# Kernel optimization log

Measured on AMD Instinct MI355X. Metric: run time of the kernel, lower is better.

The kernel has to match this reference:

```python
import jax, jax.numpy as jnp
import numpy as np

EMB_DIM = 768
N_HEAD = 12
WIN = (14, 14)  # relative_window_size; seq_len must equal 14*14=196
BATCH = 64
SEQ = WIN[0] * WIN[1]


def _relative_position_index(wh, ww):
    coords = np.stack(np.meshgrid(np.arange(wh), np.arange(ww), indexing='ij'))
    coords = coords.reshape(2, -1)
    rel = coords[:, :, None] - coords[:, None, :]          # [2, S, S]
    rel = rel.transpose(1, 2, 0).astype(np.int32)          # [S, S, 2]
    rel[:, :, 0] += wh - 1
    rel[:, :, 1] += ww - 1
    rel[:, :, 0] *= 2 * ww - 1
    return rel.sum(-1)                                     # [S, S]


def setup_inputs() -> dict:
    key = jax.random.key(0)
    ks = jax.random.split(key, 10)
    d = EMB_DIM
    std = 0.01
    x = jax.random.normal(ks[0], (BATCH, SEQ, d), dtype=jnp.float32)
    Wq = std * jax.random.normal(ks[1], (d, d), dtype=jnp.float32)
    Wk = std * jax.random.normal(ks[2], (d, d), dtype=jnp.float32)
    Wv = std * jax.random.normal(ks[3], (d, d), dtype=jnp.float32)
    Wo = std * jax.random.normal(ks[4], (d, d), dtype=jnp.float32)
    bq = jnp.zeros((d,), jnp.float32)
    bk = jnp.zeros((d,), jnp.float32)
    bv = jnp.zeros((d,), jnp.float32)
    bo = jnp.zeros((d,), jnp.float32)
    n_bias = (2 * WIN[0] - 1) * (2 * WIN[1] - 1)           # 729
    bias_table = std * jax.random.normal(ks[5], (n_bias, N_HEAD), dtype=jnp.float32)
    rel_index = jnp.asarray(_relative_position_index(WIN[0], WIN[1]))  # int32 [S,S]
    return {"x": x, "Wq": Wq, "bq": bq, "Wk": Wk, "bk": bk, "Wv": Wv,
            "bv": bv, "Wo": Wo, "bo": bo, "bias_table": bias_table,
            "rel_index": rel_index}


def reference(x, Wq, bq, Wk, bk, Wv, bv, Wo, bo, bias_table, rel_index):
    B, S, D = x.shape
    H = N_HEAD
    pd = D // H  # projection_dim

    def split_heads(t):
        return t.reshape(B, S, H, pd).transpose(0, 2, 1, 3)  # [B,H,S,pd]

    q = split_heads(x @ Wq + bq)
    k = split_heads(x @ Wk + bk)
    v = split_heads(x @ Wv + bv)

    # scores: [B,H,S,S], scaled by sqrt(projection_dim) as in the source
    score = jnp.einsum('bhqd,bhkd->bhqk', q, k) / jnp.sqrt(jnp.float32(pd))

    # Swin-style relative position bias: gather [S*S] rows -> [1,H,S,S]
    bias = bias_table[rel_index.reshape(-1)].reshape(S, S, H)
    bias = bias.transpose(2, 0, 1)[None]
    score = score + bias

    weight = jax.nn.softmax(score, axis=-1)
    out = jnp.einsum('bhqk,bhkd->bhqd', weight, v)          # [B,H,S,pd]
    out = out.transpose(0, 2, 1, 3).reshape(B, S, D)
    return out @ Wo + bo
```

## Files before the change

### kernel.cpp

```cpp
#include <hip/hip_runtime.h>
#include <hip/hip_bf16.h>


typedef __bf16 bf16x8 __attribute__((ext_vector_type(8)));
typedef __bf16 bf16x4 __attribute__((ext_vector_type(4)));
typedef float  f32x4  __attribute__((ext_vector_type(4)));

#define MROWS 12544
#define DDIM  768
#define NHEAD 12
#define SEQ   196
#define KSTR  72
#define VSTR  232

static __device__ __forceinline__ f32x4 MFMA(bf16x8 a, bf16x8 b, f32x4 c) {
    return __builtin_amdgcn_mfma_f32_16x16x32_bf16(a, b, c, 0, 0, 0);
}

static __device__ __forceinline__ void gload16(const __bf16* g, __bf16* l) {
    __builtin_amdgcn_global_load_lds(
        (const __attribute__((address_space(1))) void*)(g),
        (__attribute__((address_space(3))) void*)(l),
        16, 0, 0);
}

__global__ __launch_bounds__(256) void f2b(const float* __restrict__ in,
                                           __bf16* __restrict__ out) {
    size_t i = ((size_t)blockIdx.x * 256 + threadIdx.x) * 8;
    f32x4 a = *(const f32x4*)&in[i];
    f32x4 b = *(const f32x4*)&in[i + 4];
    bf16x8 o;
    o[0] = (__bf16)a[0]; o[1] = (__bf16)a[1]; o[2] = (__bf16)a[2]; o[3] = (__bf16)a[3];
    o[4] = (__bf16)b[0]; o[5] = (__bf16)b[1]; o[6] = (__bf16)b[2]; o[7] = (__bf16)b[3];
    *(bf16x8*)&out[i] = o;
}

__global__ __launch_bounds__(256) void wtrans(const float* __restrict__ W0, const float* __restrict__ W1,
                                              const float* __restrict__ W2, const float* __restrict__ W3,
                                              __bf16* __restrict__ T0, __bf16* __restrict__ T1,
                                              __bf16* __restrict__ T2, __bf16* __restrict__ T3) {
    const float* Ws[4] = {W0, W1, W2, W3};
    __bf16*      Ts[4] = {T0, T1, T2, T3};
    const float* W = Ws[blockIdx.z];
    __bf16*      T = Ts[blockIdx.z];
    __shared__ __bf16 t[32][33];
    int k0 = blockIdx.x * 32, n0 = blockIdx.y * 32;
    int c = threadIdx.x & 31, r = threadIdx.x >> 5;
#pragma unroll
    for (int i = 0; i < 4; ++i)
        t[r + i * 8][c] = (__bf16)W[(size_t)(k0 + r + i * 8) * DDIM + n0 + c];
    __syncthreads();
#pragma unroll
    for (int i = 0; i < 4; ++i)
        T[(size_t)(n0 + r + i * 8) * DDIM + k0 + c] = t[c][r + i * 8];
}

__global__ __launch_bounds__(256) void bias_pre(const float* __restrict__ table,
                                                const int* __restrict__ rel,
                                                __bf16* __restrict__ biasH) {
    int i = blockIdx.x * 256 + threadIdx.x;
    if (i < NHEAD * SEQ * SEQ) {
        int h = i / (SEQ * SEQ), qk = i - h * (SEQ * SEQ);
        biasH[i] = (__bf16)table[rel[qk] * NHEAD + h];
    }
}

template <typename OutT, int NMAT>
__global__ __launch_bounds__(512, 2) void gemm8p(const __bf16* __restrict__ A,
                                                 const __bf16* __restrict__ Bt,
                                                 const float* __restrict__ bz0,
                                                 const float* __restrict__ bz1,
                                                 const float* __restrict__ bz2,
                                                 OutT* __restrict__ Cz0,
                                                 OutT* __restrict__ Cz1,
                                                 OutT* __restrict__ Cz2,
                                                 int nbn) {
    __shared__ __bf16 As[3][256 * 64];
    __shared__ __bf16 Bs[2][256 * 64];

    const int nwg = gridDim.x, orig = blockIdx.x;
    const int qq = nwg >> 3, r8 = nwg & 7, xcd = orig & 7, lin = orig >> 3;
    const int wg = (xcd < r8 ? xcd * (qq + 1) : r8 * (qq + 1) + (xcd - r8) * qq) + lin;
    const int bm = wg / nbn, bn = wg - bm * nbn;
    const int m0 = bm * 256, n0g = bn * 256;

    const int tid = threadIdx.x, w = tid >> 6, l = tid & 63;
    const int lr = l & 15, lg = l >> 4;
    const int wrow = (w >> 2) * 128;
    const int wcol = (w & 3) * 64;

    const int srow = w * 8 + (l >> 3);
    const int scol = ((l & 7) ^ ((l >> 3) & 7)) * 8;
    const __bf16* gA = A  + (size_t)(m0 + srow) * DDIM + scol;
    const __bf16* gB = Bt + (size_t)(n0g + srow) * DDIM + scol;

#define STAGE_A(slot, h, kt)                                                      \
    do {                                                                          \
        gload16(gA + ((h) * 128 + 0) * DDIM + (kt) * 64,                          \
                &As[slot][(h) * 8192 + 0 + w * 512]);                             \
        gload16(gA + ((h) * 128 + 64) * DDIM + (kt) * 64,                         \
                &As[slot][(h) * 8192 + 4096 + w * 512]);                          \
    } while (0)
#define STAGE_B(slot, h, kt)                                                      \
    do {                                                                          \
        gload16(gB + ((h) * 128 + 0) * DDIM + (kt) * 64,                          \
                &Bs[slot][(h) * 8192 + 0 + w * 512]);                             \
        gload16(gB + ((h) * 128 + 64) * DDIM + (kt) * 64,                         \
                &Bs[slot][(h) * 8192 + 4096 + w * 512]);                          \
    } while (0)

#define AF(slot, mf, ks)                                                          \
    (*(const bf16x8*)&As[slot][(w >> 2) * 8192 + ((mf) * 16 + lr) * 64 +          \
                              ((((ks) * 4 + lg) ^ (lr & 7))) * 8])
#define BF(slot, nf, ks)                                                          \
    (*(const bf16x8*)&Bs[slot][((w & 3) >> 1) * 8192 +                            \
                              ((w & 1) * 64 + (nf) * 16 + lr) * 64 +              \
                              ((((ks) * 4 + lg) ^ (lr & 7))) * 8])

    f32x4 acc[8][4];
#pragma unroll
    for (int i = 0; i < 8; ++i)
#pragma unroll
        for (int j = 0; j < 4; ++j) acc[i][j] = (f32x4){0.f, 0.f, 0.f, 0.f};

    bf16x8 a0, a1, a2, a3;
    bf16x8 bfr00, bfr01, bfr10, bfr11, bfr20, bfr21, bfr30, bfr31;

#define DSLOAD_A(slot, mf0)                                                       \
    a0 = AF(slot, mf0, 0); a1 = AF(slot, mf0, 1);                                 \
    a2 = AF(slot, (mf0) + 1, 0); a3 = AF(slot, (mf0) + 1, 1);
#define DSLOAD_B(slot)                                                            \
    bfr00 = BF(slot, 0, 0); bfr01 = BF(slot, 0, 1);                               \
    bfr10 = BF(slot, 1, 0); bfr11 = BF(slot, 1, 1);                               \
    bfr20 = BF(slot, 2, 0); bfr21 = BF(slot, 2, 1);                               \
    bfr30 = BF(slot, 3, 0); bfr31 = BF(slot, 3, 1);
#define BARRIER_IN()                                                              \
    __builtin_amdgcn_sched_barrier(0);                                            \
    __builtin_amdgcn_s_barrier();                                                 \
    asm volatile("s_waitcnt lgkmcnt(0)" ::: "memory");                            \
    __builtin_amdgcn_sched_barrier(0);                                            \
    __builtin_amdgcn_s_setprio(1);
#define BARRIER_OUT()                                                             \
    __builtin_amdgcn_s_setprio(0);                                                \
    __builtin_amdgcn_sched_barrier(0);                                            \
    __builtin_amdgcn_s_barrier();                                                 \
    __builtin_amdgcn_sched_barrier(0);
#define MFMACL(mf0)                                                               \
    acc[mf0][0] = MFMA(a0, bfr00, acc[mf0][0]);                                   \
    acc[mf0][0] = MFMA(a1, bfr01, acc[mf0][0]);                                   \
    acc[(mf0) + 1][0] = MFMA(a2, bfr00, acc[(mf0) + 1][0]);                       \
    acc[(mf0) + 1][0] = MFMA(a3, bfr01, acc[(mf0) + 1][0]);                       \
    acc[mf0][1] = MFMA(a0, bfr10, acc[mf0][1]);                                   \
    acc[mf0][1] = MFMA(a1, bfr11, acc[mf0][1]);                                   \
    acc[(mf0) + 1][1] = MFMA(a2, bfr10, acc[(mf0) + 1][1]);                       \
    acc[(mf0) + 1][1] = MFMA(a3, bfr11, acc[(mf0) + 1][1]);                       \
    acc[mf0][2] = MFMA(a0, bfr20, acc[mf0][2]);                                   \
    acc[mf0][2] = MFMA(a1, bfr21, acc[mf0][2]);                                   \
    acc[(mf0) + 1][2] = MFMA(a2, bfr20, acc[(mf0) + 1][2]);                       \
    acc[(mf0) + 1][2] = MFMA(a3, bfr21, acc[(mf0) + 1][2]);                       \
    acc[mf0][3] = MFMA(a0, bfr30, acc[mf0][3]);                                   \
    acc[mf0][3] = MFMA(a1, bfr31, acc[mf0][3]);                                   \
    acc[(mf0) + 1][3] = MFMA(a2, bfr30, acc[(mf0) + 1][3]);                       \
    acc[(mf0) + 1][3] = MFMA(a3, bfr31, acc[(mf0) + 1][3]);

    STAGE_A(0, 0, 0); STAGE_A(0, 1, 0); STAGE_B(0, 0, 0); STAGE_B(0, 1, 0);
    STAGE_A(1, 0, 1); STAGE_A(1, 1, 1); STAGE_B(1, 0, 1); STAGE_B(1, 1, 1);
    asm volatile("s_waitcnt vmcnt(8)" ::: "memory");
    __builtin_amdgcn_s_barrier();
    __builtin_amdgcn_sched_barrier(0);

#pragma unroll
    for (int i = 0; i < 6; ++i) {
        const int s0 = (2 * i) % 3, s1 = (2 * i + 1) % 3, s2 = (2 * i + 2) % 3;
        DSLOAD_A(s0, 0); DSLOAD_B(0);
        if (i < 5) STAGE_A(s2, 0, 2 * i + 2);
        BARRIER_IN(); MFMACL(0); BARRIER_OUT();
        DSLOAD_A(s0, 2);
        if (i < 5) STAGE_A(s2, 1, 2 * i + 2);
        BARRIER_IN(); MFMACL(2); BARRIER_OUT();
        DSLOAD_A(s0, 4);
        if (i < 5) STAGE_B(0, 0, 2 * i + 2);
        BARRIER_IN(); MFMACL(4); BARRIER_OUT();
        DSLOAD_A(s0, 6);
        if (i < 5) {
            STAGE_B(0, 1, 2 * i + 2);
            asm volatile("s_waitcnt vmcnt(8)" ::: "memory");
        } else {
            asm volatile("s_waitcnt vmcnt(0)" ::: "memory");
        }
        BARRIER_IN(); MFMACL(6); BARRIER_OUT();
        DSLOAD_A(s1, 0); DSLOAD_B(1);
        if (i < 5) STAGE_A(s0, 0, 2 * i + 3);
        BARRIER_IN(); MFMACL(0); BARRIER_OUT();
        DSLOAD_A(s1, 2);
        if (i < 5) STAGE_A(s0, 1, 2 * i + 3);
        BARRIER_IN(); MFMACL(2); BARRIER_OUT();
        DSLOAD_A(s1, 4);
        if (i < 5) STAGE_B(1, 0, 2 * i + 3);
        BARRIER_IN(); MFMACL(4); BARRIER_OUT();
        DSLOAD_A(s1, 6);
        if (i < 5) {
            STAGE_B(1, 1, 2 * i + 3);
            asm volatile("s_waitcnt vmcnt(8)" ::: "memory");
        }
        BARRIER_IN(); MFMACL(6); BARRIER_OUT();
    }

    const int mat = (NMAT == 1) ? 0 : (n0g / DDIM);
    const int colbase = n0g - mat * DDIM + wcol;
    const float* bz = (mat == 0) ? bz0 : (mat == 1 ? bz1 : bz2);
    OutT* Cc = (mat == 0) ? Cz0 : (mat == 1 ? Cz1 : Cz2);
#pragma unroll
    for (int nf = 0; nf < 4; ++nf) {
        const int col = colbase + nf * 16 + lr;
        const float bb = bz[col];
#pragma unroll
        for (int mf = 0; mf < 8; ++mf) {
            const int row = m0 + wrow + mf * 16 + lg * 4;
#pragma unroll
            for (int r2 = 0; r2 < 4; ++r2)
                Cc[(size_t)(row + r2) * DDIM + col] = (OutT)(acc[mf][nf][r2] + bb);
        }
    }
#undef STAGE_A
#undef STAGE_B
#undef AF
#undef BF
#undef DSLOAD_A
#undef DSLOAD_B
#undef BARRIER_IN
#undef BARRIER_OUT
#undef MFMACL
}

__global__ __launch_bounds__(512, 2) void attn_kernel(const __bf16* __restrict__ Qg,
                                                      const __bf16* __restrict__ Kg,
                                                      const __bf16* __restrict__ Vg,
                                                      const __bf16* __restrict__ biasH,
                                                      __bf16* __restrict__ Og) {
    __shared__ __bf16 Ksm[208 * KSTR];
    __shared__ __bf16 Vts[64 * VSTR];
    __shared__ __bf16 Psm[8 * 16 * VSTR];

    const int b = blockIdx.x, h = blockIdx.y;
    const int tid = threadIdx.x, w = tid >> 6, l = tid & 63;
    const int lr = l & 15, lg = l >> 4;
    const size_t base = (size_t)(b * SEQ) * DDIM + h * 64;
    const __bf16* Kb = Kg + base;
    const __bf16* Vb = Vg + base;
    const __bf16* Qb = Qg + base;
    const __bf16* bh = biasH + (size_t)h * (SEQ * SEQ);

    for (int c = tid; c < SEQ * 8; c += 512) {
        int kk = c >> 3, d8 = (c & 7) << 3;
        *(bf16x8*)&Ksm[kk * KSTR + d8] = *(const bf16x8*)&Kb[(size_t)kk * DDIM + d8];
    }
    for (int c = tid; c < 12 * 9; c += 512) {
        int kk = SEQ + c / 9, d8 = (c % 9) * 8;
        *(uint4*)&Ksm[kk * KSTR + d8] = make_uint4(0u, 0u, 0u, 0u);
    }
    for (int c = tid; c < SEQ * 8; c += 512) {
        int kk = c >> 3, d8 = (c & 7) << 3;
        bf16x8 vv = *(const bf16x8*)&Vb[(size_t)kk * DDIM + d8];
#pragma unroll
        for (int j = 0; j < 8; ++j) Vts[(d8 + j) * VSTR + kk] = vv[j];
    }
    for (int c = tid; c < 64 * 28; c += 512)
        Vts[(c / 28) * VSTR + SEQ + (c % 28)] = (__bf16)0.f;
    __bf16* Pw = &Psm[w * 16 * VSTR];
    for (int c = l; c < 256; c += 64)
        Pw[(c >> 4) * VSTR + 208 + (c & 15)] = (__bf16)0.f;
    __syncthreads();

    for (int qt = w; qt < 13; qt += 8) {
        const int q0 = qt * 16;
        const int q = q0 + lr;
        const int qrow = min(q, SEQ - 1);
        bf16x8 bq0 = *(const bf16x8*)&Qb[(size_t)qrow * DDIM + lg * 8];
        bf16x8 bq1 = *(const bf16x8*)&Qb[(size_t)qrow * DDIM + 32 + lg * 8];

        f32x4 sc[13];
        __builtin_amdgcn_s_setprio(1);
#pragma unroll
        for (int t = 0; t < 13; ++t) {
            bf16x8 kf0 = *(const bf16x8*)&Ksm[(t * 16 + lr) * KSTR + lg * 8];
            bf16x8 kf1 = *(const bf16x8*)&Ksm[(t * 16 + lr) * KSTR + 32 + lg * 8];
            f32x4 a = {0.f, 0.f, 0.f, 0.f};
            a = MFMA(kf0, bq0, a);
            a = MFMA(kf1, bq1, a);
            sc[t] = a;
        }
        __builtin_amdgcn_s_setprio(0);

        float mx = -1e30f;
#pragma unroll
        for (int t = 0; t < 13; ++t) {
            const bool val4 = (t < 12) || (lg == 0);
            float bb[4] = {0.f, 0.f, 0.f, 0.f};
            if (val4) {
                bf16x4 b4 = *(const bf16x4*)&bh[(size_t)qrow * SEQ + t * 16 + lg * 4];
#pragma unroll
                for (int r = 0; r < 4; ++r) bb[r] = (float)b4[r];
            }
#pragma unroll
            for (int r = 0; r < 4; ++r) {
                float v = val4 ? (sc[t][r] * 0.125f + bb[r]) : -1e30f;
                sc[t][r] = v;
                mx = fmaxf(mx, v);
            }
        }
        mx = fmaxf(mx, __shfl_xor(mx, 16));
        mx = fmaxf(mx, __shfl_xor(mx, 32));

        float sum = 0.f;
#pragma unroll
        for (int t = 0; t < 13; ++t)
#pragma unroll
            for (int r = 0; r < 4; ++r) {
                float p = __expf(sc[t][r] - mx);
                sum += p;
                sc[t][r] = p;
            }
        sum += __shfl_xor(sum, 16);
        sum += __shfl_xor(sum, 32);
        const float inv = 1.f / sum;

#pragma unroll
        for (int t = 0; t < 13; ++t) {
            bf16x4 pk;
#pragma unroll
            for (int r = 0; r < 4; ++r) pk[r] = (__bf16)sc[t][r];
            *(bf16x4*)&Pw[lr * VSTR + t * 16 + lg * 4] = pk;
        }

        f32x4 oa[4];
#pragma unroll
        for (int i = 0; i < 4; ++i) oa[i] = (f32x4){0.f, 0.f, 0.f, 0.f};
        __builtin_amdgcn_s_setprio(1);
#pragma unroll
        for (int kt = 0; kt < 7; ++kt) {
            bf16x8 pf = *(const bf16x8*)&Pw[lr * VSTR + kt * 32 + lg * 8];
#pragma unroll
            for (int nt = 0; nt < 4; ++nt) {
                bf16x8 vf = *(const bf16x8*)&Vts[(nt * 16 + lr) * VSTR + kt * 32 + lg * 8];
                oa[nt] = MFMA(vf, pf, oa[nt]);
            }
        }
        __builtin_amdgcn_s_setprio(0);

        if (q < SEQ) {
#pragma unroll
            for (int nt = 0; nt < 4; ++nt) {
                bf16x4 ok;
#pragma unroll
                for (int r = 0; r < 4; ++r) ok[r] = (__bf16)(oa[nt][r] * inv);
                *(bf16x4*)&Og[(size_t)(b * SEQ + q) * DDIM + h * 64 + nt * 16 + lg * 4] = ok;
            }
        }
    }
}

extern "C" void kernel_launch(void* const* d_in, const int* in_sizes, int n_in,
                              void* d_out, int out_size, void* d_ws, size_t ws_size,
                              hipStream_t stream) {
    const float* x     = (const float*)d_in[0];
    const float* Wq    = (const float*)d_in[1];
    const float* bq    = (const float*)d_in[2];
    const float* Wk    = (const float*)d_in[3];
    const float* bk    = (const float*)d_in[4];
    const float* Wv    = (const float*)d_in[5];
    const float* bv    = (const float*)d_in[6];
    const float* Wo    = (const float*)d_in[7];
    const float* bo    = (const float*)d_in[8];
    const float* table = (const float*)d_in[9];
    const int*   rel   = (const int*)d_in[10];
    float* out = (float*)d_out;

    char* ws = (char*)d_ws;
    auto alloc = [&](size_t bytes) {
        char* p = ws;
        ws += (bytes + 255) & ~(size_t)255;
        return p;
    };
    const size_t mat = (size_t)MROWS * DDIM * sizeof(__bf16);
    __bf16* xb    = (__bf16*)alloc(mat);
    __bf16* Tqkv  = (__bf16*)alloc((size_t)3 * DDIM * DDIM * 2);
    __bf16* To    = (__bf16*)alloc((size_t)DDIM * DDIM * 2);
    __bf16* Qb    = (__bf16*)alloc(mat);
    __bf16* Kb    = (__bf16*)alloc(mat);
    __bf16* Vb    = (__bf16*)alloc(mat);
    __bf16* AO    = (__bf16*)alloc(mat);
    __bf16* biasH = (__bf16*)alloc((size_t)NHEAD * SEQ * SEQ * 2);

    f2b<<<dim3(4704), 256, 0, stream>>>(x, xb);
    wtrans<<<dim3(24, 24, 4), 256, 0, stream>>>(Wq, Wk, Wv, Wo,
                                                Tqkv, Tqkv + (size_t)DDIM * DDIM,
                                                Tqkv + (size_t)2 * DDIM * DDIM, To);
    bias_pre<<<dim3(1801), 256, 0, stream>>>(table, rel, biasH);

    gemm8p<__bf16, 3><<<dim3(441), 512, 0, stream>>>(xb, Tqkv, bq, bk, bv,
                                                     Qb, Kb, Vb, 9);
    attn_kernel<<<dim3(64, 12), 512, 0, stream>>>(Qb, Kb, Vb, biasH, AO);
    gemm8p<float, 1><<<dim3(147), 512, 0, stream>>>(AO, To, bo, bo, bo,
                                                    out, out, out, 3);
}
```

Measured before the change: 171.8 us.

## Split attention softmax into two online-softmax chunks and relax launch bounds

Replaces the single-pass softmax over all 13 key tiles with two chunks (8 and 5 tiles) using a running max and sum, rescaling the output accumulator between chunks. Each chunk's P tiles are written to LDS and consumed by the PV MFMAs, so fewer score registers are live at once. The launch bound minimum blocks per SM also drops from 2 to 1, giving the compiler more register headroom. The rescaling adds extra exp and multiply work and may reduce occupancy.

Result: faster. 160.2 us (-6.8%).

```diff
diff --git a/kernel.cpp b/kernel.cpp
--- a/kernel.cpp
+++ b/kernel.cpp
@@ -233,7 +233,7 @@
 #undef MFMACL
 }
 
-__global__ __launch_bounds__(512, 2) void attn_kernel(const __bf16* __restrict__ Qg,
+__global__ __launch_bounds__(512, 1) void attn_kernel(const __bf16* __restrict__ Qg,
                                                       const __bf16* __restrict__ Kg,
                                                       const __bf16* __restrict__ Vg,
                                                       const __bf16* __restrict__ biasH,
@@ -272,6 +272,77 @@
         Pw[(c >> 4) * VSTR + 208 + (c & 15)] = (__bf16)0.f;
     __syncthreads();
 
+#define CHUNK(T0, NTC, KT0, KTN)                                                  \
+    {                                                                             \
+        f32x4 sc[NTC];                                                            \
+        __builtin_amdgcn_s_setprio(1);                                            \
+        _Pragma("unroll")                                                         \
+        for (int tt = 0; tt < NTC; ++tt) {                                        \
+            const int t = (T0) + tt;                                              \
+            bf16x8 kf0 = *(const bf16x8*)&Ksm[(t * 16 + lr) * KSTR + lg * 8];     \
+            bf16x8 kf1 = *(const bf16x8*)&Ksm[(t * 16 + lr) * KSTR + 32 + lg * 8];\
+            f32x4 a = {0.f, 0.f, 0.f, 0.f};                                       \
+            a = MFMA(kf0, bq0, a);                                                \
+            a = MFMA(kf1, bq1, a);                                                \
+            sc[tt] = a;                                                           \
+        }                                                                         \
+        __builtin_amdgcn_s_setprio(0);                                            \
+        float mc = -1e30f;                                                        \
+        _Pragma("unroll")                                                         \
+        for (int tt = 0; tt < NTC; ++tt) {                                        \
+            const int t = (T0) + tt;                                              \
+            const bool val4 = (t < 12) || (lg == 0);                              \
+            float bb[4] = {0.f, 0.f, 0.f, 0.f};                                   \
+            if (val4) {                                                           \
+                bf16x4 b4 = *(const bf16x4*)&bh[(size_t)qrow * SEQ + t * 16 + lg * 4]; \
+                _Pragma("unroll")                                                 \
+                for (int r = 0; r < 4; ++r) bb[r] = (float)b4[r];                 \
+            }                                                                     \
+            _Pragma("unroll")                                                     \
+            for (int r = 0; r < 4; ++r) {                                         \
+                float v = val4 ? (sc[tt][r] * 0.125f + bb[r]) : -1e30f;           \
+                sc[tt][r] = v;                                                    \
+                mc = fmaxf(mc, v);                                                \
+            }                                                                     \
+        }                                                                         \
+        mc = fmaxf(mc, __shfl_xor(mc, 16));                                       \
+        mc = fmaxf(mc, __shfl_xor(mc, 32));                                       \
+        const float mnew = fmaxf(m_run, mc);                                      \
+        const float fsc = __expf(m_run - mnew);                                   \
+        m_run = mnew;                                                             \
+        s_run *= fsc;                                                             \
+        _Pragma("unroll")                                                         \
+        for (int i = 0; i < 4; ++i)                                               \
+            _Pragma("unroll")                                                     \
+            for (int r = 0; r < 4; ++r) oa[i][r] *= fsc;                          \
+        float ps = 0.f;                                                           \
+        _Pragma("unroll")                                                         \
+        for (int tt = 0; tt < NTC; ++tt) {                                        \
+            bf16x4 pk;                                                            \
+            _Pragma("unroll")                                                     \
+            for (int r = 0; r < 4; ++r) {                                         \
+                float p = __expf(sc[tt][r] - m_run);                              \
+                ps += p;                                                          \
+                pk[r] = (__bf16)p;                                                \
+            }                                                                     \
+            *(bf16x4*)&Pw[lr * VSTR + ((T0) + tt) * 16 + lg * 4] = pk;            \
+        }                                                                         \
+        ps += __shfl_xor(ps, 16);                                                 \
+        ps += __shfl_xor(ps, 32);                                                 \
+        s_run += ps;                                                              \
+        __builtin_amdgcn_s_setprio(1);                                            \
+        _Pragma("unroll")                                                         \
+        for (int kt = (KT0); kt < (KTN); ++kt) {                                  \
+            bf16x8 pf = *(const bf16x8*)&Pw[lr * VSTR + kt * 32 + lg * 8];        \
+            _Pragma("unroll")                                                     \
+            for (int nt = 0; nt < 4; ++nt) {                                      \
+                bf16x8 vf = *(const bf16x8*)&Vts[(nt * 16 + lr) * VSTR + kt * 32 + lg * 8]; \
+                oa[nt] = MFMA(vf, pf, oa[nt]);                                    \
+            }                                                                     \
+        }                                                                         \
+        __builtin_amdgcn_s_setprio(0);                                            \
+    }
+
     for (int qt = w; qt < 13; qt += 8) {
         const int q0 = qt * 16;
         const int q = q0 + lr;
@@ -279,75 +350,15 @@
         bf16x8 bq0 = *(const bf16x8*)&Qb[(size_t)qrow * DDIM + lg * 8];
         bf16x8 bq1 = *(const bf16x8*)&Qb[(size_t)qrow * DDIM + 32 + lg * 8];
 
-        f32x4 sc[13];
-        __builtin_amdgcn_s_setprio(1);
-#pragma unroll
-        for (int t = 0; t < 13; ++t) {
-            bf16x8 kf0 = *(const bf16x8*)&Ksm[(t * 16 + lr) * KSTR + lg * 8];
-            bf16x8 kf1 = *(const bf16x8*)&Ksm[(t * 16 + lr) * KSTR + 32 + lg * 8];
-            f32x4 a = {0.f, 0.f, 0.f, 0.f};
-            a = MFMA(kf0, bq0, a);
-            a = MFMA(kf1, bq1, a);
-            sc[t] = a;
-        }
-        __builtin_amdgcn_s_setprio(0);
-
-        float mx = -1e30f;
-#pragma unroll
-        for (int t = 0; t < 13; ++t) {
-            const bool val4 = (t < 12) || (lg == 0);
-            float bb[4] = {0.f, 0.f, 0.f, 0.f};
-            if (val4) {
-                bf16x4 b4 = *(const bf16x4*)&bh[(size_t)qrow * SEQ + t * 16 + lg * 4];
-#pragma unroll
-                for (int r = 0; r < 4; ++r) bb[r] = (float)b4[r];
-            }
-#pragma unroll
-            for (int r = 0; r < 4; ++r) {
-                float v = val4 ? (sc[t][r] * 0.125f + bb[r]) : -1e30f;
-                sc[t][r] = v;
-                mx = fmaxf(mx, v);
-            }
-        }
-        mx = fmaxf(mx, __shfl_xor(mx, 16));
-        mx = fmaxf(mx, __shfl_xor(mx, 32));
-
-        float sum = 0.f;
-#pragma unroll
-        for (int t = 0; t < 13; ++t)
-#pragma unroll
-            for (int r = 0; r < 4; ++r) {
-                float p = __expf(sc[t][r] - mx);
-                sum += p;
-                sc[t][r] = p;
-            }
-        sum += __shfl_xor(sum, 16);
-        sum += __shfl_xor(sum, 32);
-        const float inv = 1.f / sum;
-
-#pragma unroll
-        for (int t = 0; t < 13; ++t) {
-            bf16x4 pk;
-#pragma unroll
-            for (int r = 0; r < 4; ++r) pk[r] = (__bf16)sc[t][r];
-            *(bf16x4*)&Pw[lr * VSTR + t * 16 + lg * 4] = pk;
-        }
-
+        float m_run = -1e30f, s_run = 0.f;
         f32x4 oa[4];
 #pragma unroll
         for (int i = 0; i < 4; ++i) oa[i] = (f32x4){0.f, 0.f, 0.f, 0.f};
-        __builtin_amdgcn_s_setprio(1);
-#pragma unroll
-        for (int kt = 0; kt < 7; ++kt) {
-            bf16x8 pf = *(const bf16x8*)&Pw[lr * VSTR + kt * 32 + lg * 8];
-#pragma unroll
-            for (int nt = 0; nt < 4; ++nt) {
-                bf16x8 vf = *(const bf16x8*)&Vts[(nt * 16 + lr) * VSTR + kt * 32 + lg * 8];
-                oa[nt] = MFMA(vf, pf, oa[nt]);
-            }
-        }
-        __builtin_amdgcn_s_setprio(0);
-
+
+        CHUNK(0, 8, 0, 4);
+        CHUNK(8, 5, 4, 7);
+
+        const float inv = 1.f / s_run;
         if (q < SEQ) {
 #pragma unroll
             for (int nt = 0; nt < 4; ++nt) {
@@ -358,6 +369,7 @@
             }
         }
     }
+#undef CHUNK
 }
 
 extern "C" void kernel_launch(void* const* d_in, const int* in_sizes, int n_in,
```

## Chunk attention softmax online to cut registers and LDS, raise occupancy

Applied to the files above, without the earlier changes.

Splits the per-query-tile score computation into four key chunks processed with an online (running max/sum) softmax, so only 4 score tiles stay live instead of 13. The P staging buffer shrinks to a 64-wide stride and the K stride drops to 68, reducing LDS per block. Launch bounds move to 4 blocks per SM to exploit the lower register and LDS footprint. This adds rescaling work (extra exps and multiplies per chunk) and changes the K padding stride, which may alter LDS bank-conflict behavior.

New measurement: 265.9 us. +54.8%, slower.

```diff
diff --git a/kernel.cpp b/kernel.cpp
--- a/kernel.cpp
+++ b/kernel.cpp
@@ -10,8 +10,9 @@
 #define DDIM  768
 #define NHEAD 12
 #define SEQ   196
-#define KSTR  72
+#define KSTR  68
 #define VSTR  232
+#define PSTR  68
 
 static __device__ __forceinline__ f32x4 MFMA(bf16x8 a, bf16x8 b, f32x4 c) {
     return __builtin_amdgcn_mfma_f32_16x16x32_bf16(a, b, c, 0, 0, 0);
@@ -233,14 +234,92 @@
 #undef MFMACL
 }
 
-__global__ __launch_bounds__(512, 2) void attn_kernel(const __bf16* __restrict__ Qg,
+template <int T0, int NTC, int KT0, int NKT, bool REZERO>
+static __device__ __forceinline__ void attn_chunk(
+    const __bf16* Ksm, const __bf16* Vts, __bf16* Pw, const __bf16* bh,
+    int qrow, int lr, int lg, bf16x8 bq0, bf16x8 bq1,
+    float& m_run, float& s_run, f32x4* oa) {
+    f32x4 sc[NTC];
+    __builtin_amdgcn_s_setprio(1);
+#pragma unroll
+    for (int tt = 0; tt < NTC; ++tt) {
+        const int t = T0 + tt;
+        bf16x8 kf0 = *(const bf16x8*)&Ksm[(t * 16 + lr) * KSTR + lg * 8];
+        bf16x8 kf1 = *(const bf16x8*)&Ksm[(t * 16 + lr) * KSTR + 32 + lg * 8];
+        f32x4 a = {0.f, 0.f, 0.f, 0.f};
+        a = MFMA(kf0, bq0, a);
+        a = MFMA(kf1, bq1, a);
+        sc[tt] = a;
+    }
+    __builtin_amdgcn_s_setprio(0);
+    float mc = -1e30f;
+#pragma unroll
+    for (int tt = 0; tt < NTC; ++tt) {
+        const int t = T0 + tt;
+        const bool val4 = (t < 12) || (lg == 0);
+        float bb[4] = {0.f, 0.f, 0.f, 0.f};
+        if (val4) {
+            bf16x4 b4 = *(const bf16x4*)&bh[(size_t)qrow * SEQ + t * 16 + lg * 4];
+#pragma unroll
+            for (int r = 0; r < 4; ++r) bb[r] = (float)b4[r];
+        }
+#pragma unroll
+        for (int r = 0; r < 4; ++r) {
+            float v = val4 ? (sc[tt][r] * 0.125f + bb[r]) : -1e30f;
+            sc[tt][r] = v;
+            mc = fmaxf(mc, v);
+        }
+    }
+    mc = fmaxf(mc, __shfl_xor(mc, 16));
+    mc = fmaxf(mc, __shfl_xor(mc, 32));
+    const float mnew = fmaxf(m_run, mc);
+    const float fsc = __expf(m_run - mnew);
+    m_run = mnew;
+    s_run *= fsc;
+#pragma unroll
+    for (int i = 0; i < 4; ++i)
+#pragma unroll
+        for (int r = 0; r < 4; ++r) oa[i][r] *= fsc;
+    float ps = 0.f;
+#pragma unroll
+    for (int tt = 0; tt < NTC; ++tt) {
+        bf16x4 pk;
+#pragma unroll
+        for (int r = 0; r < 4; ++r) {
+            float p = __expf(sc[tt][r] - m_run);
+            ps += p;
+            pk[r] = (__bf16)p;
+        }
+        *(bf16x4*)&Pw[lr * PSTR + tt * 16 + lg * 4] = pk;
+    }
+    ps += __shfl_xor(ps, 16);
+    ps += __shfl_xor(ps, 32);
+    s_run += ps;
+    if (REZERO) {
+        bf16x4 z4 = {(__bf16)0.f, (__bf16)0.f, (__bf16)0.f, (__bf16)0.f};
+        *(bf16x4*)&Pw[lr * PSTR + 16 + lg * 4] = z4;
+    }
+    __builtin_amdgcn_s_setprio(1);
+#pragma unroll
+    for (int ktl = 0; ktl < NKT; ++ktl) {
+        bf16x8 pf = *(const bf16x8*)&Pw[lr * PSTR + ktl * 32 + lg * 8];
+#pragma unroll
+        for (int nt = 0; nt < 4; ++nt) {
+            bf16x8 vf = *(const bf16x8*)&Vts[(nt * 16 + lr) * VSTR + (KT0 + ktl) * 32 + lg * 8];
+            oa[nt] = MFMA(vf, pf, oa[nt]);
+        }
+    }
+    __builtin_amdgcn_s_setprio(0);
+}
+
+__global__ __launch_bounds__(512, 4) void attn_kernel(const __bf16* __restrict__ Qg,
                                                       const __bf16* __restrict__ Kg,
                                                       const __bf16* __restrict__ Vg,
                                                       const __bf16* __restrict__ biasH,
                                                       __bf16* __restrict__ Og) {
     __shared__ __bf16 Ksm[208 * KSTR];
     __shared__ __bf16 Vts[64 * VSTR];
-    __shared__ __bf16 Psm[8 * 16 * VSTR];
+    __shared__ __bf16 Psm[8 * 16 * PSTR];
 
     const int b = blockIdx.x, h = blockIdx.y;
     const int tid = threadIdx.x, w = tid >> 6, l = tid & 63;
@@ -255,8 +334,8 @@
         int kk = c >> 3, d8 = (c & 7) << 3;
         *(bf16x8*)&Ksm[kk * KSTR + d8] = *(const bf16x8*)&Kb[(size_t)kk * DDIM + d8];
     }
-    for (int c = tid; c < 12 * 9; c += 512) {
-        int kk = SEQ + c / 9, d8 = (c % 9) * 8;
+    for (int c = tid; c < 12 * 8; c += 512) {
+        int kk = SEQ + (c >> 3), d8 = (c & 7) << 3;
         *(uint4*)&Ksm[kk * KSTR + d8] = make_uint4(0u, 0u, 0u, 0u);
     }
     for (int c = tid; c < SEQ * 8; c += 512) {
@@ -267,10 +346,9 @@
     }
     for (int c = tid; c < 64 * 28; c += 512)
         Vts[(c / 28) * VSTR + SEQ + (c % 28)] = (__bf16)0.f;
-    __bf16* Pw = &Psm[w * 16 * VSTR];
-    for (int c = l; c < 256; c += 64)
-        Pw[(c >> 4) * VSTR + 208 + (c & 15)] = (__bf16)0.f;
     __syncthreads();
+
+    __bf16* Pw = &Psm[w * 16 * PSTR];
 
     for (int qt = w; qt < 13; qt += 8) {
         const int q0 = qt * 16;
@@ -279,75 +357,17 @@
         bf16x8 bq0 = *(const bf16x8*)&Qb[(size_t)qrow * DDIM + lg * 8];
         bf16x8 bq1 = *(const bf16x8*)&Qb[(size_t)qrow * DDIM + 32 + lg * 8];
 
-        f32x4 sc[13];
-        __builtin_amdgcn_s_setprio(1);
-#pragma unroll
-        for (int t = 0; t < 13; ++t) {
-            bf16x8 kf0 = *(const bf16x8*)&Ksm[(t * 16 + lr) * KSTR + lg * 8];
-            bf16x8 kf1 = *(const bf16x8*)&Ksm[(t * 16 + lr) * KSTR + 32 + lg * 8];
-            f32x4 a = {0.f, 0.f, 0.f, 0.f};
-            a = MFMA(kf0, bq0, a);
-            a = MFMA(kf1, bq1, a);
-            sc[t] = a;
-        }
-        __builtin_amdgcn_s_setprio(0);
-
-        float mx = -1e30f;
-#pragma unroll
-        for (int t = 0; t < 13; ++t) {
-            const bool val4 = (t < 12) || (lg == 0);
-            float bb[4] = {0.f, 0.f, 0.f, 0.f};
-            if (val4) {
-                bf16x4 b4 = *(const bf16x4*)&bh[(size_t)qrow * SEQ + t * 16 + lg * 4];
-#pragma unroll
-                for (int r = 0; r < 4; ++r) bb[r] = (float)b4[r];
-            }
-#pragma unroll
-            for (int r = 0; r < 4; ++r) {
-                float v = val4 ? (sc[t][r] * 0.125f + bb[r]) : -1e30f;
-                sc[t][r] = v;
-                mx = fmaxf(mx, v);
-            }
-        }
-        mx = fmaxf(mx, __shfl_xor(mx, 16));
-        mx = fmaxf(mx, __shfl_xor(mx, 32));
-
-        float sum = 0.f;
-#pragma unroll
-        for (int t = 0; t < 13; ++t)
-#pragma unroll
-            for (int r = 0; r < 4; ++r) {
-                float p = __expf(sc[t][r] - mx);
-                sum += p;
-                sc[t][r] = p;
-            }
-        sum += __shfl_xor(sum, 16);
-        sum += __shfl_xor(sum, 32);
-        const float inv = 1.f / sum;
-
-#pragma unroll
-        for (int t = 0; t < 13; ++t) {
-            bf16x4 pk;
-#pragma unroll
-            for (int r = 0; r < 4; ++r) pk[r] = (__bf16)sc[t][r];
-            *(bf16x4*)&Pw[lr * VSTR + t * 16 + lg * 4] = pk;
-        }
-
+        float m_run = -1e30f, s_run = 0.f;
         f32x4 oa[4];
 #pragma unroll
         for (int i = 0; i < 4; ++i) oa[i] = (f32x4){0.f, 0.f, 0.f, 0.f};
-        __builtin_amdgcn_s_setprio(1);
-#pragma unroll
-        for (int kt = 0; kt < 7; ++kt) {
-            bf16x8 pf = *(const bf16x8*)&Pw[lr * VSTR + kt * 32 + lg * 8];
-#pragma unroll
-            for (int nt = 0; nt < 4; ++nt) {
-                bf16x8 vf = *(const bf16x8*)&Vts[(nt * 16 + lr) * VSTR + kt * 32 + lg * 8];
-                oa[nt] = MFMA(vf, pf, oa[nt]);
-            }
-        }
-        __builtin_amdgcn_s_setprio(0);
-
+
+        attn_chunk<0, 4, 0, 2, false>(Ksm, Vts, Pw, bh, qrow, lr, lg, bq0, bq1, m_run, s_run, oa);
+        attn_chunk<4, 4, 2, 2, false>(Ksm, Vts, Pw, bh, qrow, lr, lg, bq0, bq1, m_run, s_run, oa);
+        attn_chunk<8, 4, 4, 2, false>(Ksm, Vts, Pw, bh, qrow, lr, lg, bq0, bq1, m_run, s_run, oa);
+        attn_chunk<12, 1, 6, 1, true>(Ksm, Vts, Pw, bh, qrow, lr, lg, bq0, bq1, m_run, s_run, oa);
+
+        const float inv = 1.f / s_run;
         if (q < SEQ) {
 #pragma unroll
             for (int nt = 0; nt < 4; ++nt) {
```

## Split attention softmax into two online-softmax chunks to overlap exp with PV MFMA

Applied to the files above, without the earlier changes.

Restructures the per-query-tile attention so the 13 key tiles are processed in two chunks (8 and 5) with online-softmax rescaling. The first chunk's probabilities feed the PV MFMAs while the second chunk's scores and exponentials are computed. The aim is to interleave VALU exp work with matrix work and shrink live score registers. It also relaxes launch bounds from 2 to 1 waves per SIMD hint, which allows more registers but may lower occupancy, and adds rescale overhead.

New measurement: 161.2 us. -6.2%, faster.

```diff
diff --git a/kernel.cpp b/kernel.cpp
--- a/kernel.cpp
+++ b/kernel.cpp
@@ -233,7 +233,7 @@
 #undef MFMACL
 }
 
-__global__ __launch_bounds__(512, 2) void attn_kernel(const __bf16* __restrict__ Qg,
+__global__ __launch_bounds__(512, 1) void attn_kernel(const __bf16* __restrict__ Qg,
                                                       const __bf16* __restrict__ Kg,
                                                       const __bf16* __restrict__ Vg,
                                                       const __bf16* __restrict__ biasH,
@@ -279,22 +279,71 @@
         bf16x8 bq0 = *(const bf16x8*)&Qb[(size_t)qrow * DDIM + lg * 8];
         bf16x8 bq1 = *(const bf16x8*)&Qb[(size_t)qrow * DDIM + 32 + lg * 8];
 
-        f32x4 sc[13];
+        f32x4 oa[4];
+#pragma unroll
+        for (int i = 0; i < 4; ++i) oa[i] = (f32x4){0.f, 0.f, 0.f, 0.f};
+
+        f32x4 sc1[8];
         __builtin_amdgcn_s_setprio(1);
 #pragma unroll
-        for (int t = 0; t < 13; ++t) {
+        for (int tt = 0; tt < 8; ++tt) {
+            bf16x8 kf0 = *(const bf16x8*)&Ksm[(tt * 16 + lr) * KSTR + lg * 8];
+            bf16x8 kf1 = *(const bf16x8*)&Ksm[(tt * 16 + lr) * KSTR + 32 + lg * 8];
+            f32x4 a = {0.f, 0.f, 0.f, 0.f};
+            a = MFMA(kf0, bq0, a);
+            a = MFMA(kf1, bq1, a);
+            sc1[tt] = a;
+        }
+        __builtin_amdgcn_s_setprio(0);
+
+        float mx = -1e30f;
+#pragma unroll
+        for (int tt = 0; tt < 8; ++tt) {
+            bf16x4 b4 = *(const bf16x4*)&bh[(size_t)qrow * SEQ + tt * 16 + lg * 4];
+#pragma unroll
+            for (int r = 0; r < 4; ++r) {
+                float v = sc1[tt][r] * 0.125f + (float)b4[r];
+                sc1[tt][r] = v;
+                mx = fmaxf(mx, v);
+            }
+        }
+        mx = fmaxf(mx, __shfl_xor(mx, 16));
+        mx = fmaxf(mx, __shfl_xor(mx, 32));
+        float m_run = mx;
+        float ps = 0.f;
+#pragma unroll
+        for (int tt = 0; tt < 8; ++tt) {
+            bf16x4 pk;
+#pragma unroll
+            for (int r = 0; r < 4; ++r) {
+                float p = __expf(sc1[tt][r] - m_run);
+                ps += p;
+                pk[r] = (__bf16)p;
+            }
+            *(bf16x4*)&Pw[lr * VSTR + tt * 16 + lg * 4] = pk;
+        }
+        ps += __shfl_xor(ps, 16);
+        ps += __shfl_xor(ps, 32);
+        float s_run = ps;
+
+        f32x4 sc2[5];
+        __builtin_amdgcn_s_setprio(1);
+#pragma unroll
+        for (int tt = 0; tt < 5; ++tt) {
+            const int t = 8 + tt;
             bf16x8 kf0 = *(const bf16x8*)&Ksm[(t * 16 + lr) * KSTR + lg * 8];
             bf16x8 kf1 = *(const bf16x8*)&Ksm[(t * 16 + lr) * KSTR + 32 + lg * 8];
             f32x4 a = {0.f, 0.f, 0.f, 0.f};
             a = MFMA(kf0, bq0, a);
             a = MFMA(kf1, bq1, a);
-            sc[t] = a;
+            sc2[tt] = a;
         }
         __builtin_amdgcn_s_setprio(0);
 
-        float mx = -1e30f;
-#pragma unroll
-        for (int t = 0; t < 13; ++t) {
+        float mc2 = -1e30f;
+#pragma unroll
+        for (int tt = 0; tt < 5; ++tt) {
+            const int t = 8 + tt;
             const bool val4 = (t < 12) || (lg == 0);
             float bb[4] = {0.f, 0.f, 0.f, 0.f};
             if (val4) {
@@ -304,41 +353,17 @@
             }
 #pragma unroll
             for (int r = 0; r < 4; ++r) {
-                float v = val4 ? (sc[t][r] * 0.125f + bb[r]) : -1e30f;
-                sc[t][r] = v;
-                mx = fmaxf(mx, v);
-            }
-        }
-        mx = fmaxf(mx, __shfl_xor(mx, 16));
-        mx = fmaxf(mx, __shfl_xor(mx, 32));
-
-        float sum = 0.f;
-#pragma unroll
-        for (int t = 0; t < 13; ++t)
-#pragma unroll
-            for (int r = 0; r < 4; ++r) {
-                float p = __expf(sc[t][r] - mx);
-                sum += p;
-                sc[t][r] = p;
-            }
-        sum += __shfl_xor(sum, 16);
-        sum += __shfl_xor(sum, 32);
-        const float inv = 1.f / sum;
-
-#pragma unroll
-        for (int t = 0; t < 13; ++t) {
-            bf16x4 pk;
-#pragma unroll
-            for (int r = 0; r < 4; ++r) pk[r] = (__bf16)sc[t][r];
-            *(bf16x4*)&Pw[lr * VSTR + t * 16 + lg * 4] = pk;
-        }
-
-        f32x4 oa[4];
-#pragma unroll
-        for (int i = 0; i < 4; ++i) oa[i] = (f32x4){0.f, 0.f, 0.f, 0.f};
+                float v = val4 ? (sc2[tt][r] * 0.125f + bb[r]) : -1e30f;
+                sc2[tt][r] = v;
+                mc2 = fmaxf(mc2, v);
+            }
+        }
+        mc2 = fmaxf(mc2, __shfl_xor(mc2, 16));
+        mc2 = fmaxf(mc2, __shfl_xor(mc2, 32));
+
         __builtin_amdgcn_s_setprio(1);
 #pragma unroll
-        for (int kt = 0; kt < 7; ++kt) {
+        for (int kt = 0; kt < 4; ++kt) {
             bf16x8 pf = *(const bf16x8*)&Pw[lr * VSTR + kt * 32 + lg * 8];
 #pragma unroll
             for (int nt = 0; nt < 4; ++nt) {
@@ -348,6 +373,43 @@
         }
         __builtin_amdgcn_s_setprio(0);
 
+        const float mnew = fmaxf(m_run, mc2);
+        const float fsc = __expf(m_run - mnew);
+        m_run = mnew;
+        s_run *= fsc;
+#pragma unroll
+        for (int i = 0; i < 4; ++i)
+#pragma unroll
+            for (int r = 0; r < 4; ++r) oa[i][r] *= fsc;
+        ps = 0.f;
+#pragma unroll
+        for (int tt = 0; tt < 5; ++tt) {
+            bf16x4 pk;
+#pragma unroll
+            for (int r = 0; r < 4; ++r) {
+                float p = __expf(sc2[tt][r] - m_run);
+                ps += p;
+                pk[r] = (__bf16)p;
+            }
+            *(bf16x4*)&Pw[lr * VSTR + (8 + tt) * 16 + lg * 4] = pk;
+        }
+        ps += __shfl_xor(ps, 16);
+        ps += __shfl_xor(ps, 32);
+        s_run += ps;
+
+        __builtin_amdgcn_s_setprio(1);
+#pragma unroll
+        for (int kt = 4; kt < 7; ++kt) {
+            bf16x8 pf = *(const bf16x8*)&Pw[lr * VSTR + kt * 32 + lg * 8];
+#pragma unroll
+            for (int nt = 0; nt < 4; ++nt) {
+                bf16x8 vf = *(const bf16x8*)&Vts[(nt * 16 + lr) * VSTR + kt * 32 + lg * 8];
+                oa[nt] = MFMA(vf, pf, oa[nt]);
+            }
+        }
+        __builtin_amdgcn_s_setprio(0);
+
+        const float inv = 1.f / s_run;
         if (q < SEQ) {
 #pragma unroll
             for (int nt = 0; nt < 4; ++nt) {
```
